# Performance work log

Hardware: AMD Instinct MI355X
Metric: run time of the kernel (lower is better)

## Reference

```python
import jax, jax.numpy as jnp
import numpy as np

N = 100000      # nodes
E = 1600000     # edges (avg degree 16)
DIN = 128
DOUT = 128


def setup_inputs() -> dict:
    key = jax.random.key(0)
    k1, k2, k3, k4 = jax.random.split(key, 4)
    x = jax.random.normal(k1, (N, DIN), dtype=jnp.float32)
    edge_index = jax.random.randint(k2, (2, E), 0, N, dtype=jnp.int64)
    # guarantee every node appears at least once as a source row so that
    # degree > 0 everywhere (1/sqrt(0) would be inf, as in the torch code)
    row = edge_index[0].at[:N].set(jnp.arange(N, dtype=jnp.int64))
    edge_index = jnp.stack([row, edge_index[1]])
    W = jax.random.normal(k3, (DOUT, DIN), dtype=jnp.float32) / np.sqrt(DIN)
    b = jax.random.normal(k4, (DOUT,), dtype=jnp.float32) * 0.01
    return {"x": x, "edge_index": edge_index, "W": W, "b": b}


def reference(x, edge_index, W, b):
    # Math identical to: A = dense(add_self_loops(edge_index));
    # D = 1/sqrt(degree(edge_index[0]))  (degree WITHOUT self-loops);
    # out = (D_i * A_ij * D_j) @ (x W^T + b)
    row, col = edge_index[0], edge_index[1]
    deg = jax.ops.segment_sum(jnp.ones(row.shape[0], x.dtype), row, num_segments=N)
    d = jax.lax.rsqrt(deg)                      # [N]
    h = x @ W.T + b                             # [N, DOUT]
    # edge contributions: out[r] += D[r] * D[c] * h[c]  (duplicate edges sum, as to_dense does)
    agg = jax.ops.segment_sum(d[col][:, None] * h[col], row, num_segments=N)
    # self-loop term added for every node: D[i]^2 * h[i]
    out = d[:, None] * agg + (d * d)[:, None] * h
    return out
```

## Files before the change

kernel.cpp:

```cpp
#include <hip/hip_runtime.h>

#define D 128
#define BROWS 512
#define LOGB 9
#define NBMAX 256
#define CHUNK 4096
#define SCAP 10240
#define NCHMAX 512
#define LDSW 136

typedef __attribute__((ext_vector_type(8))) short bf16x8;
typedef __attribute__((ext_vector_type(4))) float f32x4;

__device__ inline unsigned short f2bf(float f) {
    unsigned u = __float_as_uint(f);
    u += 0x7FFFu + ((u >> 16) & 1u);
    return (unsigned short)(u >> 16);
}
__device__ inline float bf2f(unsigned short h) {
    return __uint_as_float((unsigned)h << 16);
}
__device__ inline float bflo(unsigned u) { return __uint_as_float(u << 16); }
__device__ inline float bfhi(unsigned u) { return __uint_as_float(u & 0xFFFF0000u); }

__global__ __launch_bounds__(512) void k_bin(const int* __restrict__ row,
                                             const int* __restrict__ col,
                                             int E, unsigned* __restrict__ ebuf,
                                             int* __restrict__ sc_g,
                                             const float* __restrict__ W,
                                             unsigned short* __restrict__ Wbh,
                                             unsigned short* __restrict__ Wbl) {
    __shared__ int lhist[NBMAX];
    __shared__ int sc[NBMAX];
    __shared__ unsigned sstage[CHUNK];
    int t = threadIdx.x;
    if (blockIdx.x < 8) {
        int wb = blockIdx.x * 2048 + t;
        #pragma unroll
        for (int i = 0; i < 4; ++i) {
            int idx = wb + i * 512;
            float wv = W[idx];
            unsigned short h = f2bf(wv);
            Wbh[idx] = h;
            Wbl[idx] = f2bf(wv - bf2f(h));
        }
    }
    int base = blockIdx.x * CHUNK;
    if (t < NBMAX) lhist[t] = 0;
    __syncthreads();
    int b[8], p[8]; unsigned pk[8];
    #pragma unroll
    for (int i = 0; i < 8; ++i) {
        int idx = base + i * 512 + t;
        if (idx < E) {
            int r = row[idx], c = col[idx];
            b[i] = r >> LOGB;
            pk[i] = ((unsigned)(r & (BROWS - 1)) << 17) | (unsigned)c;
            p[i] = atomicAdd(&lhist[b[i]], 1);
        } else b[i] = -1;
    }
    __syncthreads();
    if (t < 64) {
        int a0 = lhist[4*t], a1 = lhist[4*t+1], a2 = lhist[4*t+2], a3 = lhist[4*t+3];
        int s = a0 + a1 + a2 + a3;
        int incl = s;
        #pragma unroll
        for (int m = 1; m < 64; m <<= 1) {
            int tmp = __shfl_up(incl, m);
            if (t >= m) incl += tmp;
        }
        int excl = incl - s;
        sc[4*t] = excl; sc[4*t+1] = excl + a0;
        sc[4*t+2] = excl + a0 + a1; sc[4*t+3] = excl + a0 + a1 + a2;
    }
    __syncthreads();
    int total = sc[NBMAX - 1] + lhist[NBMAX - 1];
    #pragma unroll
    for (int i = 0; i < 8; ++i)
        if (b[i] >= 0) sstage[sc[b[i]] + p[i]] = pk[i];
    if (t < 257) sc_g[blockIdx.x * 257 + t] = (t < 256) ? sc[t] : total;
    __syncthreads();
    for (int i = t; i < total; i += 512)
        ebuf[base + i] = sstage[i];
}

__global__ __launch_bounds__(1024) void k_group(const int* __restrict__ sc_g,
                                                const unsigned* __restrict__ ebuf,
                                                int N, int NBK, int NCH,
                                                float* __restrict__ dvals,
                                                int* __restrict__ rptr,
                                                int* __restrict__ csr_col,
                                                unsigned short* __restrict__ Hs) {
    __shared__ unsigned sebuf[SCAP];
    __shared__ int lhist[BROWS];
    __shared__ int chS[NCHMAX], chO[NCHMAX], chL[NCHMAX];
    __shared__ int wtot[16], woff[16];
    __shared__ int sEbase, sCnt;
    int bkt = blockIdx.x, t = threadIdx.x;
    int lane = t & 63, wv = t >> 6;

    int s0 = 0, len = 0;
    if (t < NCH) {
        s0 = sc_g[t * 257 + bkt];
        len = sc_g[t * 257 + bkt + 1] - s0;
    }
    if (t == 0) sEbase = 0;
    if (t < BROWS) lhist[t] = 0;
    __syncthreads();
    if (t < NCH) { chS[t] = s0; atomicAdd(&sEbase, s0); }
    int incl = len;
    #pragma unroll
    for (int m = 1; m < 64; m <<= 1) {
        int tmp = __shfl_up(incl, m);
        if (lane >= m) incl += tmp;
    }
    if (lane == 63) wtot[wv] = incl;
    __syncthreads();
    if (t < 16) {
        int w = wtot[t];
        int wincl = w;
        #pragma unroll
        for (int m = 1; m < 16; m <<= 1) {
            int tmp = __shfl_up(wincl, m);
            if (t >= m) wincl += tmp;
        }
        woff[t] = wincl - w;
        if (t == 15) sCnt = wincl;
    }
    __syncthreads();
    if (t < NCH) {
        int off = woff[wv] + incl - len;
        int l = len;
        if (off > SCAP) off = SCAP;
        if (off + l > SCAP) l = SCAP - off;
        chO[t] = off;
        chL[t] = l;
    }
    __syncthreads();
    for (int ch = wv; ch < NCH; ch += 16) {
        int so = chS[ch], off = chO[ch], l = chL[ch];
        for (int b0 = 0; b0 < l; b0 += 64) {
            int k = b0 + lane;
            if (k < l) sebuf[off + k] = ebuf[(size_t)ch * CHUNK + so + k];
        }
    }
    __syncthreads();
    int cnt = sCnt; if (cnt > SCAP) cnt = SCAP;
    for (int i = t; i < cnt; i += 1024)
        atomicAdd(&lhist[sebuf[i] >> 17], 1);
    __syncthreads();
    int v = 0, incl2 = 0;
    if (t < BROWS) {
        v = lhist[t];
        incl2 = v;
        #pragma unroll
        for (int m = 1; m < 64; m <<= 1) {
            int tmp = __shfl_up(incl2, m);
            if (lane >= m) incl2 += tmp;
        }
        if (lane == 63) wtot[wv] = incl2;
    }
    __syncthreads();
    if (t < 8) {
        int w = wtot[t];
        int wincl = w;
        #pragma unroll
        for (int m = 1; m < 8; m <<= 1) {
            int tmp = __shfl_up(wincl, m);
            if (t >= m) wincl += tmp;
        }
        woff[t] = wincl - w;
    }
    __syncthreads();
    int ebase = sEbase;
    if (t < BROWS) {
        int excl = woff[wv] + incl2 - v;
        int r = (bkt << LOGB) + t;
        if (r < N) {
            rptr[r] = ebase + excl;
            dvals[r] = rsqrtf((float)v);
        }
        lhist[t] = excl;
    }
    if (bkt == NBK - 1 && t == 0) rptr[N] = ebase + cnt;
    if (bkt == 0 && t == 0) dvals[N] = 0.f;
    if (bkt == 0 && t < 64)
        ((unsigned*)(Hs + (size_t)N * D))[t] = 0u;
    __syncthreads();
    for (int i = t; i < cnt; i += 1024) {
        unsigned e = sebuf[i];
        int rr = (int)(e >> 17);
        int p = atomicAdd(&lhist[rr], 1);
        csr_col[ebase + p] = (int)(e & 0x1FFFFu);
    }
}

__global__ __launch_bounds__(256, 2) void k_gc(const float* __restrict__ x,
                                               const unsigned short* __restrict__ Wbh,
                                               const unsigned short* __restrict__ Wbl,
                                               const float* __restrict__ b,
                                               const float* __restrict__ dvals,
                                               unsigned short* __restrict__ Hs, int N) {
    __shared__ unsigned short Whi[128 * LDSW];
    __shared__ unsigned short Wlo[128 * LDSW];
    __shared__ float bs[D];
    int t = threadIdx.x;
    #pragma unroll
    for (int i = 0; i < 16; ++i) {
        int idx4 = i * 256 + t;
        int r = idx4 >> 5;
        int c = (idx4 & 31) * 4;
        ((ushort4*)&Whi[r * LDSW + c])[0] = ((const ushort4*)Wbh)[idx4];
        ((ushort4*)&Wlo[r * LDSW + c])[0] = ((const ushort4*)Wbl)[idx4];
    }
    if (t < D) bs[t] = b[t];
    __syncthreads();

    int wave = t >> 6, lane = t & 63;
    int quad = lane >> 4, mrow = lane & 15;
    int row_base = blockIdx.x * 128 + wave * 32;

    bf16x8 Ahi[2][4], Alo[2][4];
    #pragma unroll
    for (int s = 0; s < 2; ++s) {
        int grow = row_base + s * 16 + mrow;
        bool ok = grow < N;
        const float* xrow = x + (size_t)(ok ? grow : 0) * D;
        #pragma unroll
        for (int kk = 0; kk < 4; ++kk) {
            int k0 = kk * 32 + quad * 8;
            float4 f0 = ok ? ((const float4*)(xrow + k0))[0] : make_float4(0, 0, 0, 0);
            float4 f1 = ok ? ((const float4*)(xrow + k0))[1] : make_float4(0, 0, 0, 0);
            float fv[8] = {f0.x, f0.y, f0.z, f0.w, f1.x, f1.y, f1.z, f1.w};
            #pragma unroll
            for (int j = 0; j < 8; ++j) {
                unsigned short h = f2bf(fv[j]);
                Ahi[s][kk][j] = (short)h;
                Alo[s][kk][j] = (short)f2bf(fv[j] - bf2f(h));
            }
        }
    }

    f32x4 acc[2][8];
    #pragma unroll
    for (int s = 0; s < 2; ++s)
        #pragma unroll
        for (int ct = 0; ct < 8; ++ct)
            acc[s][ct] = (f32x4){0.f, 0.f, 0.f, 0.f};

    #pragma unroll
    for (int ct = 0; ct < 8; ++ct) {
        int wrow = ct * 16 + mrow;
        #pragma unroll
        for (int kk = 0; kk < 4; ++kk) {
            int off = wrow * LDSW + kk * 32 + quad * 8;
            bf16x8 Bhi = *(const bf16x8*)&Whi[off];
            bf16x8 Blo = *(const bf16x8*)&Wlo[off];
            #pragma unroll
            for (int s = 0; s < 2; ++s) {
                acc[s][ct] = __builtin_amdgcn_mfma_f32_16x16x32_bf16(Ahi[s][kk], Bhi, acc[s][ct], 0, 0, 0);
                acc[s][ct] = __builtin_amdgcn_mfma_f32_16x16x32_bf16(Alo[s][kk], Bhi, acc[s][ct], 0, 0, 0);
                acc[s][ct] = __builtin_amdgcn_mfma_f32_16x16x32_bf16(Ahi[s][kk], Blo, acc[s][ct], 0, 0, 0);
            }
        }
    }

    __syncthreads();
    unsigned short* stage = Whi;
    #pragma unroll
    for (int s = 0; s < 2; ++s) {
        #pragma unroll
        for (int r = 0; r < 4; ++r) {
            int grow = row_base + s * 16 + quad * 4 + r;
            float dv = dvals[(grow < N) ? grow : N];
            int lrow = wave * 32 + s * 16 + quad * 4 + r;
            #pragma unroll
            for (int ct = 0; ct < 8; ++ct) {
                int col = ct * 16 + mrow;
                stage[lrow * LDSW + col] = f2bf(dv * (acc[s][ct][r] + bs[col]));
            }
        }
    }
    __syncthreads();
    for (int i = t; i < 128 * 16; i += 256) {
        int lrow = i >> 4;
        int g = i & 15;
        int grow = blockIdx.x * 128 + lrow;
        if (grow < N)
            ((uint4*)Hs)[(size_t)grow * 16 + g] =
                ((const uint4*)&stage[lrow * LDSW])[g];
    }
}

#define ACC8(v) do { \
    a[0] += bflo((v).x); a[1] += bfhi((v).x); \
    a[2] += bflo((v).y); a[3] += bfhi((v).y); \
    a[4] += bflo((v).z); a[5] += bfhi((v).z); \
    a[6] += bflo((v).w); a[7] += bfhi((v).w); } while (0)

__global__ __launch_bounds__(256) void k_rows(const unsigned short* __restrict__ Hs,
                                              const int* __restrict__ rptr,
                                              const int* __restrict__ csr_col,
                                              const float* __restrict__ dvals,
                                              float* __restrict__ out, int N) {
    int wid = (blockIdx.x * blockDim.x + threadIdx.x) >> 6;
    if (wid >= N) return;
    int lane = threadIdx.x & 63;
    int grp = lane >> 4, sl = lane & 15;
    int s = rptr[wid];
    int n = rptr[wid + 1] - s;
    const uint4* hv = (const uint4*)Hs;

    int cc = csr_col[s + lane];
    int ccreg = (lane < n) ? cc : N;
    uint4 vself = hv[(size_t)wid * 16 + sl];

    float a[8] = {0.f, 0.f, 0.f, 0.f, 0.f, 0.f, 0.f, 0.f};
    int nf = (n < 64) ? n : 64;

    int c0 = __shfl(ccreg, grp);
    int c1 = __shfl(ccreg, grp + 4);
    int c2 = __shfl(ccreg, grp + 8);
    int c3 = __shfl(ccreg, grp + 12);
    uint4 p0 = hv[(size_t)c0 * 16 + sl];
    uint4 p1 = hv[(size_t)c1 * 16 + sl];
    uint4 p2 = hv[(size_t)c2 * 16 + sl];
    uint4 p3 = hv[(size_t)c3 * 16 + sl];

    for (int k0 = 16; k0 < nf; k0 += 16) {
        int i0 = k0 + grp;
        int d0 = __shfl(ccreg, i0);
        int d1 = __shfl(ccreg, i0 + 4);
        int d2 = __shfl(ccreg, i0 + 8);
        int d3 = __shfl(ccreg, i0 + 12);
        uint4 q0 = hv[(size_t)d0 * 16 + sl];
        uint4 q1 = hv[(size_t)d1 * 16 + sl];
        uint4 q2 = hv[(size_t)d2 * 16 + sl];
        uint4 q3 = hv[(size_t)d3 * 16 + sl];
        ACC8(p0); ACC8(p1); ACC8(p2); ACC8(p3);
        p0 = q0; p1 = q1; p2 = q2; p3 = q3;
    }
    ACC8(p0); ACC8(p1); ACC8(p2); ACC8(p3);

    if (__builtin_expect(n > 64, 0)) {
        for (int idx = 64 + grp; idx < n; idx += 4) {
            int c = csr_col[s + idx];
            uint4 v = hv[(size_t)c * 16 + sl];
            ACC8(v);
        }
    }
    if (grp == 0) ACC8(vself);

    #pragma unroll
    for (int j = 0; j < 8; ++j) {
        a[j] += __shfl_xor(a[j], 16);
        a[j] += __shfl_xor(a[j], 32);
    }
    float dr = dvals[wid];
    if (grp < 2) {
        float4 o = (grp == 0) ? make_float4(a[0], a[1], a[2], a[3])
                              : make_float4(a[4], a[5], a[6], a[7]);
        o.x *= dr; o.y *= dr; o.z *= dr; o.w *= dr;
        ((float4*)(out + (size_t)wid * D))[sl * 2 + grp] = o;
    }
}

extern "C" void kernel_launch(void* const* d_in, const int* in_sizes, int n_in,
                              void* d_out, int out_size, void* d_ws, size_t ws_size,
                              hipStream_t stream) {
    const float* x  = (const float*)d_in[0];
    const int*   ei = (const int*)d_in[1];
    const float* W  = (const float*)d_in[2];
    const float* b  = (const float*)d_in[3];
    float* out = (float*)d_out;
    int N = in_sizes[0] / D;
    int E = in_sizes[1] / 2;
    int NB = (N + BROWS - 1) / BROWS;
    int NCH = (E + CHUNK - 1) / CHUNK;

    int*            rptr    = (int*)d_ws;
    float*          dvals   = (float*)(rptr + N + 1);
    int*            csr_col = (int*)(dvals + N + 1);
    unsigned*       ebuf    = (unsigned*)(csr_col + E + 64);
    int*            sc_g    = (int*)(ebuf + (size_t)NCH * CHUNK);
    unsigned short* Wbh     = (unsigned short*)(sc_g + (size_t)NCH * 257);
    unsigned short* Wbl     = Wbh + D * D;
    uintptr_t hs_addr = (uintptr_t)(Wbl + D * D);
    hs_addr = (hs_addr + 15) & ~(uintptr_t)15;
    unsigned short* Hs = (unsigned short*)hs_addr;

    k_bin<<<NCH, 512, 0, stream>>>(ei, ei + E, E, ebuf, sc_g, W, Wbh, Wbl);
    k_group<<<NB, 1024, 0, stream>>>(sc_g, ebuf, N, NB, NCH, dvals, rptr, csr_col, Hs);
    k_gc<<<(N + 127) / 128, 256, 0, stream>>>(x, Wbh, Wbl, b, dvals, Hs, N);
    k_rows<<<(N + 3) / 4, 256, 0, stream>>>(Hs, rptr, csr_col, dvals, out, N);
}
```

Measured before the change: 236.8 us.

## Fuse CSR grouping and dense transform into a single kernel

Merges the bucket-grouping kernel and the MFMA-based x·W^T transform into one kernel. Each grouping block then computes H for its own 512 rows, reusing the shared-memory buffer and taking degree scales from LDS instead of global memory. This removes one kernel launch and the dvals round trip. In exchange, the GEMM now runs on far fewer, larger blocks with heavy LDS use, which reduces occupancy and parallelism for the memory-bound x read.

```diff
diff --git a/kernel.cpp b/kernel.cpp
--- a/kernel.cpp
+++ b/kernel.cpp
@@ -84,20 +84,27 @@
         ebuf[base + i] = sstage[i];
 }
 
-__global__ __launch_bounds__(1024) void k_group(const int* __restrict__ sc_g,
-                                                const unsigned* __restrict__ ebuf,
-                                                int N, int NBK, int NCH,
-                                                float* __restrict__ dvals,
-                                                int* __restrict__ rptr,
-                                                int* __restrict__ csr_col,
-                                                unsigned short* __restrict__ Hs) {
-    __shared__ unsigned sebuf[SCAP];
+__global__ __launch_bounds__(1024) void k_gs(const int* __restrict__ sc_g,
+                                             const unsigned* __restrict__ ebuf,
+                                             const float* __restrict__ x,
+                                             const unsigned short* __restrict__ Wbh,
+                                             const unsigned short* __restrict__ Wbl,
+                                             const float* __restrict__ bias,
+                                             int N, int NBK, int NCH,
+                                             float* __restrict__ dvals,
+                                             int* __restrict__ rptr,
+                                             int* __restrict__ csr_col,
+                                             unsigned short* __restrict__ Hs) {
+    __shared__ __align__(16) unsigned char smem[139264];
     __shared__ int lhist[BROWS];
+    __shared__ float sdl[BROWS];
     __shared__ int chS[NCHMAX], chO[NCHMAX], chL[NCHMAX];
     __shared__ int wtot[16], woff[16];
     __shared__ int sEbase, sCnt;
+    __shared__ float bs[D];
     int bkt = blockIdx.x, t = threadIdx.x;
     int lane = t & 63, wv = t >> 6;
+    unsigned* sebuf = (unsigned*)smem;
 
     int s0 = 0, len = 0;
     if (t < NCH) {
@@ -117,14 +124,14 @@
     if (lane == 63) wtot[wv] = incl;
     __syncthreads();
     if (t < 16) {
-        int w = wtot[t];
-        int wincl = w;
+        int w0 = wtot[t];
+        int wincl = w0;
         #pragma unroll
         for (int m = 1; m < 16; m <<= 1) {
             int tmp = __shfl_up(wincl, m);
             if (t >= m) wincl += tmp;
         }
-        woff[t] = wincl - w;
+        woff[t] = wincl - w0;
         if (t == 15) sCnt = wincl;
     }
     __syncthreads();
@@ -162,24 +169,26 @@
     }
     __syncthreads();
     if (t < 8) {
-        int w = wtot[t];
-        int wincl = w;
+        int w0 = wtot[t];
+        int wincl = w0;
         #pragma unroll
         for (int m = 1; m < 8; m <<= 1) {
             int tmp = __shfl_up(wincl, m);
             if (t >= m) wincl += tmp;
         }
-        woff[t] = wincl - w;
+        woff[t] = wincl - w0;
     }
     __syncthreads();
     int ebase = sEbase;
     if (t < BROWS) {
         int excl = woff[wv] + incl2 - v;
         int r = (bkt << LOGB) + t;
+        float dl = rsqrtf((float)v);
         if (r < N) {
             rptr[r] = ebase + excl;
-            dvals[r] = rsqrtf((float)v);
-        }
+            dvals[r] = dl;
+        }
+        sdl[t] = dl;
         lhist[t] = excl;
     }
     if (bkt == NBK - 1 && t == 0) rptr[N] = ebase + cnt;
@@ -193,39 +202,29 @@
         int p = atomicAdd(&lhist[rr], 1);
         csr_col[ebase + p] = (int)(e & 0x1FFFFu);
     }
-}
-
-__global__ __launch_bounds__(256, 2) void k_gc(const float* __restrict__ x,
-                                               const unsigned short* __restrict__ Wbh,
-                                               const unsigned short* __restrict__ Wbl,
-                                               const float* __restrict__ b,
-                                               const float* __restrict__ dvals,
-                                               unsigned short* __restrict__ Hs, int N) {
-    __shared__ unsigned short Whi[128 * LDSW];
-    __shared__ unsigned short Wlo[128 * LDSW];
-    __shared__ float bs[D];
-    int t = threadIdx.x;
-    #pragma unroll
-    for (int i = 0; i < 16; ++i) {
-        int idx4 = i * 256 + t;
+    __syncthreads();
+
+    unsigned short* Whi = (unsigned short*)smem;
+    unsigned short* Wlo = (unsigned short*)(smem + 34816);
+    unsigned short* stage = (unsigned short*)(smem + 69632);
+    #pragma unroll
+    for (int i = 0; i < 4; ++i) {
+        int idx4 = i * 1024 + t;
         int r = idx4 >> 5;
         int c = (idx4 & 31) * 4;
         ((ushort4*)&Whi[r * LDSW + c])[0] = ((const ushort4*)Wbh)[idx4];
         ((ushort4*)&Wlo[r * LDSW + c])[0] = ((const ushort4*)Wbl)[idx4];
     }
-    if (t < D) bs[t] = b[t];
-    __syncthreads();
-
-    int wave = t >> 6, lane = t & 63;
-    int quad = lane >> 4, mrow = lane & 15;
-    int row_base = blockIdx.x * 128 + wave * 32;
-
-    bf16x8 Ahi[2][4], Alo[2][4];
-    #pragma unroll
-    for (int s = 0; s < 2; ++s) {
-        int grow = row_base + s * 16 + mrow;
+    if (t < D) bs[t] = bias[t];
+    __syncthreads();
+
+    int w = wv, quad = lane >> 4, mrow = lane & 15;
+    for (int p = 0; p < 2; ++p) {
+        int rowbase = (bkt << LOGB) + p * 256 + w * 16;
+        int grow = rowbase + mrow;
         bool ok = grow < N;
         const float* xrow = x + (size_t)(ok ? grow : 0) * D;
+        bf16x8 Ahi[4], Alo[4];
         #pragma unroll
         for (int kk = 0; kk < 4; ++kk) {
             int k0 = kk * 32 + quad * 8;
@@ -235,60 +234,46 @@
             #pragma unroll
             for (int j = 0; j < 8; ++j) {
                 unsigned short h = f2bf(fv[j]);
-                Ahi[s][kk][j] = (short)h;
-                Alo[s][kk][j] = (short)f2bf(fv[j] - bf2f(h));
+                Ahi[kk][j] = (short)h;
+                Alo[kk][j] = (short)f2bf(fv[j] - bf2f(h));
             }
         }
-    }
-
-    f32x4 acc[2][8];
-    #pragma unroll
-    for (int s = 0; s < 2; ++s)
-        #pragma unroll
-        for (int ct = 0; ct < 8; ++ct)
-            acc[s][ct] = (f32x4){0.f, 0.f, 0.f, 0.f};
-
-    #pragma unroll
-    for (int ct = 0; ct < 8; ++ct) {
-        int wrow = ct * 16 + mrow;
-        #pragma unroll
-        for (int kk = 0; kk < 4; ++kk) {
-            int off = wrow * LDSW + kk * 32 + quad * 8;
-            bf16x8 Bhi = *(const bf16x8*)&Whi[off];
-            bf16x8 Blo = *(const bf16x8*)&Wlo[off];
+        f32x4 acc[8];
+        #pragma unroll
+        for (int ct = 0; ct < 8; ++ct) acc[ct] = (f32x4){0.f, 0.f, 0.f, 0.f};
+        #pragma unroll
+        for (int ct = 0; ct < 8; ++ct) {
+            int wrow = ct * 16 + mrow;
             #pragma unroll
-            for (int s = 0; s < 2; ++s) {
-                acc[s][ct] = __builtin_amdgcn_mfma_f32_16x16x32_bf16(Ahi[s][kk], Bhi, acc[s][ct], 0, 0, 0);
-                acc[s][ct] = __builtin_amdgcn_mfma_f32_16x16x32_bf16(Alo[s][kk], Bhi, acc[s][ct], 0, 0, 0);
-                acc[s][ct] = __builtin_amdgcn_mfma_f32_16x16x32_bf16(Ahi[s][kk], Blo, acc[s][ct], 0, 0, 0);
+            for (int kk = 0; kk < 4; ++kk) {
+                int off = wrow * LDSW + kk * 32 + quad * 8;
+                bf16x8 Bhi = *(const bf16x8*)&Whi[off];
+                bf16x8 Blo = *(const bf16x8*)&Wlo[off];
+                acc[ct] = __builtin_amdgcn_mfma_f32_16x16x32_bf16(Ahi[kk], Bhi, acc[ct], 0, 0, 0);
+                acc[ct] = __builtin_amdgcn_mfma_f32_16x16x32_bf16(Alo[kk], Bhi, acc[ct], 0, 0, 0);
+                acc[ct] = __builtin_amdgcn_mfma_f32_16x16x32_bf16(Ahi[kk], Blo, acc[ct], 0, 0, 0);
             }
         }
-    }
-
-    __syncthreads();
-    unsigned short* stage = Whi;
-    #pragma unroll
-    for (int s = 0; s < 2; ++s) {
-        #pragma unroll
-        for (int r = 0; r < 4; ++r) {
-            int grow = row_base + s * 16 + quad * 4 + r;
-            float dv = dvals[(grow < N) ? grow : N];
-            int lrow = wave * 32 + s * 16 + quad * 4 + r;
+        #pragma unroll
+        for (int r2 = 0; r2 < 4; ++r2) {
+            int lrow = w * 16 + quad * 4 + r2;
+            int gr = (bkt << LOGB) + p * 256 + lrow;
+            float dv = (gr < N) ? sdl[p * 256 + lrow] : 0.f;
             #pragma unroll
             for (int ct = 0; ct < 8; ++ct) {
                 int col = ct * 16 + mrow;
-                stage[lrow * LDSW + col] = f2bf(dv * (acc[s][ct][r] + bs[col]));
+                stage[lrow * LDSW + col] = f2bf(dv * (acc[ct][r2] + bs[col]));
             }
         }
-    }
-    __syncthreads();
-    for (int i = t; i < 128 * 16; i += 256) {
-        int lrow = i >> 4;
-        int g = i & 15;
-        int grow = blockIdx.x * 128 + lrow;
-        if (grow < N)
-            ((uint4*)Hs)[(size_t)grow * 16 + g] =
-                ((const uint4*)&stage[lrow * LDSW])[g];
+        __syncthreads();
+        for (int i = t; i < 256 * 16; i += 1024) {
+            int lrow = i >> 4, g = i & 15;
+            int gr = (bkt << LOGB) + p * 256 + lrow;
+            if (gr < N)
+                ((uint4*)Hs)[(size_t)gr * 16 + g] =
+                    ((const uint4*)&stage[lrow * LDSW])[g];
+        }
+        __syncthreads();
     }
 }
 
@@ -345,8 +330,8 @@
     if (__builtin_expect(n > 64, 0)) {
         for (int idx = 64 + grp; idx < n; idx += 4) {
             int c = csr_col[s + idx];
-            uint4 v = hv[(size_t)c * 16 + sl];
-            ACC8(v);
+            uint4 vv = hv[(size_t)c * 16 + sl];
+            ACC8(vv);
         }
     }
     if (grp == 0) ACC8(vself);
@@ -390,7 +375,7 @@
     unsigned short* Hs = (unsigned short*)hs_addr;
 
     k_bin<<<NCH, 512, 0, stream>>>(ei, ei + E, E, ebuf, sc_g, W, Wbh, Wbl);
-    k_group<<<NB, 1024, 0, stream>>>(sc_g, ebuf, N, NB, NCH, dvals, rptr, csr_col, Hs);
-    k_gc<<<(N + 127) / 128, 256, 0, stream>>>(x, Wbh, Wbl, b, dvals, Hs, N);
+    k_gs<<<NB, 1024, 0, stream>>>(sc_g, ebuf, x, Wbh, Wbl, b, N, NB, NCH,
+                                  dvals, rptr, csr_col, Hs);
     k_rows<<<(N + 3) / 4, 256, 0, stream>>>(Hs, rptr, csr_col, dvals, out, N);
 }
```

New measurement: 230.3 us. 1.03x faster.
